# Kernel tuning notes

Measured on AMD Instinct MI355X. Metric: run time of the kernel, lower is better.

Reference implementation:

```python
import jax, jax.numpy as jnp
import numpy as np

N_NODES = 50000

def setup_inputs() -> dict:
    key = jax.random.key(0)
    k1, k2, k3, k4, k5 = jax.random.split(key, 5)
    feat = jax.random.normal(k1, (N_NODES, 192), dtype=jnp.float32)
    edge_feat = jax.random.normal(k2, (800000, 64), dtype=jnp.float32)
    src = jax.random.randint(k3, (800000,), 0, N_NODES, dtype=jnp.int32)
    dst = jax.random.randint(k4, (800000,), 0, N_NODES, dtype=jnp.int32)
    weight = jax.random.normal(k5, (256, 256), dtype=jnp.float32) * (1.0 / np.sqrt(256.0))
    bias = jnp.zeros((256,), dtype=jnp.float32)
    return {"feat": feat, "edge_feat": edge_feat, "src": src, "dst": dst,
            "weight": weight, "bias": bias}


def reference(feat, edge_feat, src, dst, weight, bias):
    N = feat.shape[0]
    ones_e = jnp.ones(src.shape[0], dtype=jnp.float32)
    # out-degree normalization of source features (pre-aggregation)
    out_deg = jnp.clip(jax.ops.segment_sum(ones_e, src, num_segments=N), 1.0, None)
    feat_n = feat * (out_deg ** -0.5)[:, None]            # [N, d_node]
    # message = concat(src_feat_norm, edge_feat); sum over dst.
    # segment_sum distributes over concat, so aggregate parts separately
    # (avoids materializing the [E, d_node+d_edge] message tensor).
    h_src = jax.ops.segment_sum(feat_n[src], dst, num_segments=N)   # [N, d_node]
    h_edge = jax.ops.segment_sum(edge_feat, dst, num_segments=N)    # [N, d_edge]
    h = jnp.concatenate([h_src, h_edge], axis=1)          # [N, in_feats]
    rst = h @ weight                                      # [N, out_feats]
    # in-degree normalization (post-aggregation)
    in_deg = jnp.clip(jax.ops.segment_sum(ones_e, dst, num_segments=N), 1.0, None)
    rst = rst * (in_deg ** -0.5)[:, None] + bias
    return rst
```

## Files before the change

### kernel.cpp

```cpp
#include <hip/hip_runtime.h>

#define NN 50000
#define NE 800000
#define DIN 256
#define DOUT 256

typedef __attribute__((ext_vector_type(8))) short bf16x8;
typedef __attribute__((ext_vector_type(8))) unsigned short u16x8;
typedef __attribute__((ext_vector_type(4))) float f32x4;

__device__ __forceinline__ unsigned short f2bf(float x) {
    unsigned int u = __builtin_bit_cast(unsigned int, x);
    u += 0x7fffu + ((u >> 16) & 1u);
    return (unsigned short)(u >> 16);
}
__device__ __forceinline__ float bf2f(unsigned short b) {
    return __builtin_bit_cast(float, ((unsigned int)b) << 16);
}


__global__ __launch_bounds__(256) void zero_meta(int* __restrict__ p, int n) {
    int i = blockIdx.x * 256 + threadIdx.x;
    if (i < n) p[i] = 0;
}

__global__ __launch_bounds__(256) void count_kernel(const int* __restrict__ src,
                                                    const int* __restrict__ dst,
                                                    int* __restrict__ in_cnt,
                                                    int* __restrict__ out_cnt) {
    int e = blockIdx.x * 256 + threadIdx.x;
    if (e < NE) {
        atomicAdd(in_cnt + dst[e], 1);
        atomicAdd(out_cnt + src[e], 1);
    }
}

__global__ __launch_bounds__(256) void scan1(const int* __restrict__ cnt,
                                             int* __restrict__ row_off,
                                             int* __restrict__ bsum) {
    __shared__ int tmp[256];
    int tid = threadIdx.x;
    int i = blockIdx.x * 256 + tid;
    int v = (i < NN) ? cnt[i] : 0;
    tmp[tid] = v;
    __syncthreads();
#pragma unroll
    for (int off = 1; off < 256; off <<= 1) {
        int t = (tid >= off) ? tmp[tid - off] : 0;
        __syncthreads();
        if (tid >= off) tmp[tid] += t;
        __syncthreads();
    }
    if (i < NN) row_off[i] = tmp[tid] - v;
    if (tid == 255) bsum[blockIdx.x] = tmp[255];
}

__global__ __launch_bounds__(256) void scan2(int* __restrict__ bsum, int nb) {
    __shared__ int tmp[256];
    int tid = threadIdx.x;
    int v = (tid < nb) ? bsum[tid] : 0;
    tmp[tid] = v;
    __syncthreads();
#pragma unroll
    for (int off = 1; off < 256; off <<= 1) {
        int t = (tid >= off) ? tmp[tid - off] : 0;
        __syncthreads();
        if (tid >= off) tmp[tid] += t;
        __syncthreads();
    }
    if (tid < nb) bsum[tid] = tmp[tid] - v;
}

__global__ __launch_bounds__(256) void scan3(int* __restrict__ row_off,
                                             int* __restrict__ cursor,
                                             float* __restrict__ odeg_inv,
                                             const int* __restrict__ out_cnt,
                                             const int* __restrict__ bsum) {
    int i = blockIdx.x * 256 + threadIdx.x;
    if (i < NN) {
        int v = row_off[i] + bsum[i >> 8];
        row_off[i] = v;
        cursor[i] = v;
        odeg_inv[i] = rsqrtf((float)max(out_cnt[i], 1));
    }
    if (i == NN) row_off[NN] = NE;
}

__global__ __launch_bounds__(256) void wconv(const float* __restrict__ W,
                                             unsigned short* __restrict__ wt) {
    int n = blockIdx.x, k = threadIdx.x;
    wt[n * 256 + k] = f2bf(W[k * 256 + n]);
}

__global__ __launch_bounds__(256) void featconv(const float* __restrict__ feat,
                                                const float* __restrict__ odeg_inv,
                                                unsigned short* __restrict__ featn) {
    int node = blockIdx.x * 4 + (threadIdx.x >> 6);
    int lane = threadIdx.x & 63;
    if (node >= NN || lane >= 48) return;
    float s = odeg_inv[node];
    float4 v = *(const float4*)(feat + (size_t)node * 192 + lane * 4);
    ushort4 o;
    o.x = f2bf(v.x * s); o.y = f2bf(v.y * s);
    o.z = f2bf(v.z * s); o.w = f2bf(v.w * s);
    *(ushort4*)(featn + (size_t)node * 192 + lane * 4) = o;
}

__global__ __launch_bounds__(256) void fill_kernel(const int* __restrict__ src,
                                                   const int* __restrict__ dst,
                                                   int* __restrict__ cursor,
                                                   int* __restrict__ perm,
                                                   unsigned short* __restrict__ eperm,
                                                   const float* __restrict__ edge_feat) {
    int tid = threadIdx.x;
    int e   = blockIdx.x * 16 + (tid >> 4);
    int sub = tid & 15;
    if (e >= NE) return;
    int pos = 0;
    if (sub == 0) {
        pos = atomicAdd(cursor + dst[e], 1);
        perm[pos] = src[e];
    }
    pos = __shfl(pos, 0, 16);
    float4 v = *(const float4*)(edge_feat + (size_t)e * 64 + sub * 4);
    ushort4 o;
    o.x = f2bf(v.x); o.y = f2bf(v.y); o.z = f2bf(v.z); o.w = f2bf(v.w);
    *(ushort4*)(eperm + (size_t)pos * 64 + sub * 4) = o;
}

__global__ __launch_bounds__(256) void aggregate_kernel(const unsigned short* __restrict__ featn,
                                                        const unsigned short* __restrict__ eperm,
                                                        const int* __restrict__ row_off,
                                                        const int* __restrict__ perm,
                                                        unsigned short* __restrict__ h_bf) {
    int node = blockIdx.x * 4 + (threadIdx.x >> 6);
    int lane = threadIdx.x & 63;
    if (node >= NN) return;
    int start = row_off[node];
    int end   = row_off[node + 1];

    int half = lane >> 5;
    int l    = lane & 31;
    bool isF = (l < 24);
    const unsigned short* fbase = featn + l * 8;
    const unsigned short* ebase = eperm + (l - 24) * 8;

    float acc[8];
#pragma unroll
    for (int k = 0; k < 8; ++k) acc[k] = 0.f;

    for (int i = start + half; i < end; i += 8) {
        int idx[4]; float w[4]; int s[4];
#pragma unroll
        for (int j = 0; j < 4; ++j) {
            int ii = i + 2 * j;
            idx[j] = min(ii, end - 1);
            w[j] = (ii < end) ? 1.f : 0.f;
        }
#pragma unroll
        for (int j = 0; j < 4; ++j) s[j] = perm[idx[j]];
        bf16x8 u[4];
#pragma unroll
        for (int j = 0; j < 4; ++j) {
            const unsigned short* p = isF ? (fbase + (size_t)s[j] * 192)
                                          : (ebase + (size_t)idx[j] * 64);
            u[j] = *(const bf16x8*)p;
        }
#pragma unroll
        for (int j = 0; j < 4; ++j) {
#pragma unroll
            for (int k = 0; k < 8; ++k)
                acc[k] = fmaf(bf2f((unsigned short)u[j][k]), w[j], acc[k]);
        }
    }

#pragma unroll
    for (int k = 0; k < 8; ++k) acc[k] += __shfl_xor(acc[k], 32);

    if (lane < 32) {
        u16x8 o;
#pragma unroll
        for (int k = 0; k < 8; ++k) o[k] = f2bf(acc[k]);
        *(u16x8*)(h_bf + (size_t)node * 256 + l * 8) = o;
    }
}

__global__ __launch_bounds__(256) void fill_fb(const int* __restrict__ src,
                                               const int* __restrict__ dst,
                                               int* __restrict__ cursor,
                                               int2* __restrict__ perm2) {
    int e = blockIdx.x * 256 + threadIdx.x;
    if (e < NE) {
        int d = dst[e];
        int pos = atomicAdd(cursor + d, 1);
        perm2[pos] = make_int2(e, src[e]);
    }
}

__global__ __launch_bounds__(256) void aggregate_fb(const unsigned short* __restrict__ featn,
                                                    const float* __restrict__ edge_feat,
                                                    const int* __restrict__ row_off,
                                                    const int2* __restrict__ perm2,
                                                    unsigned short* __restrict__ h_bf) {
    int node = blockIdx.x * 4 + (threadIdx.x >> 6);
    int lane = threadIdx.x & 63;
    if (node >= NN) return;
    int start = row_off[node];
    int end   = row_off[node + 1];

    float4 acc = make_float4(0.f, 0.f, 0.f, 0.f);

    if (lane < 48) {
        const unsigned short* fb = featn + lane * 4;
        for (int i = start; i < end; i += 8) {
            int2 p[8];
#pragma unroll
            for (int j = 0; j < 8; ++j) p[j] = perm2[min(i + j, end - 1)];
            ushort4 u[8];
#pragma unroll
            for (int j = 0; j < 8; ++j)
                u[j] = *(const ushort4*)(fb + (size_t)p[j].y * 192);
#pragma unroll
            for (int j = 0; j < 8; ++j) {
                float w = (i + j < end) ? 1.f : 0.f;
                acc.x = fmaf(bf2f(u[j].x), w, acc.x);
                acc.y = fmaf(bf2f(u[j].y), w, acc.y);
                acc.z = fmaf(bf2f(u[j].z), w, acc.z);
                acc.w = fmaf(bf2f(u[j].w), w, acc.w);
            }
        }
    } else {
        const float* eb = edge_feat + (lane - 48) * 4;
        for (int i = start; i < end; i += 8) {
            int2 p[8];
#pragma unroll
            for (int j = 0; j < 8; ++j) p[j] = perm2[min(i + j, end - 1)];
            float4 v[8];
#pragma unroll
            for (int j = 0; j < 8; ++j)
                v[j] = *(const float4*)(eb + (size_t)p[j].x * 64);
#pragma unroll
            for (int j = 0; j < 8; ++j) {
                float w = (i + j < end) ? 1.f : 0.f;
                acc.x = fmaf(v[j].x, w, acc.x);
                acc.y = fmaf(v[j].y, w, acc.y);
                acc.z = fmaf(v[j].z, w, acc.z);
                acc.w = fmaf(v[j].w, w, acc.w);
            }
        }
    }

    ushort4 o;
    o.x = f2bf(acc.x); o.y = f2bf(acc.y);
    o.z = f2bf(acc.z); o.w = f2bf(acc.w);
    *(ushort4*)(h_bf + (size_t)node * 256 + lane * 4) = o;
}

__global__ __launch_bounds__(256) void gemm_mfma(const unsigned short* __restrict__ h_bf,
                                                 const unsigned short* __restrict__ wt_bf,
                                                 const float* __restrict__ bias,
                                                 const int* __restrict__ row_off,
                                                 float* __restrict__ out) {
    int wave = threadIdx.x >> 6;
    int lane = threadIdx.x & 63;
    int m16  = lane & 15;
    int quad = lane >> 4;
    int rbase = blockIdx.x * 16;
    int cbase = wave * 64;

    const unsigned short* arow = h_bf + (size_t)(rbase + m16) * 256 + quad * 8;
    const unsigned short* b0p = wt_bf + (size_t)(cbase +  0 + m16) * 256 + quad * 8;
    const unsigned short* b1p = wt_bf + (size_t)(cbase + 16 + m16) * 256 + quad * 8;
    const unsigned short* b2p = wt_bf + (size_t)(cbase + 32 + m16) * 256 + quad * 8;
    const unsigned short* b3p = wt_bf + (size_t)(cbase + 48 + m16) * 256 + quad * 8;

    f32x4 acc0 = {0.f, 0.f, 0.f, 0.f};
    f32x4 acc1 = {0.f, 0.f, 0.f, 0.f};
    f32x4 acc2 = {0.f, 0.f, 0.f, 0.f};
    f32x4 acc3 = {0.f, 0.f, 0.f, 0.f};

#pragma unroll
    for (int k0 = 0; k0 < 256; k0 += 32) {
        bf16x8 a  = *(const bf16x8*)(arow + k0);
        bf16x8 b0 = *(const bf16x8*)(b0p + k0);
        bf16x8 b1 = *(const bf16x8*)(b1p + k0);
        bf16x8 b2 = *(const bf16x8*)(b2p + k0);
        bf16x8 b3 = *(const bf16x8*)(b3p + k0);
        acc0 = __builtin_amdgcn_mfma_f32_16x16x32_bf16(a, b0, acc0, 0, 0, 0);
        acc1 = __builtin_amdgcn_mfma_f32_16x16x32_bf16(a, b1, acc1, 0, 0, 0);
        acc2 = __builtin_amdgcn_mfma_f32_16x16x32_bf16(a, b2, acc2, 0, 0, 0);
        acc3 = __builtin_amdgcn_mfma_f32_16x16x32_bf16(a, b3, acc3, 0, 0, 0);
    }

    int grow0 = rbase + quad * 4;
    float s[4];
    int ro_prev = row_off[grow0];
#pragma unroll
    for (int r = 0; r < 4; ++r) {
        int nx = row_off[grow0 + r + 1];
        s[r] = rsqrtf((float)max(nx - ro_prev, 1));
        ro_prev = nx;
    }

    float bv0 = bias[cbase +  0 + m16];
    float bv1 = bias[cbase + 16 + m16];
    float bv2 = bias[cbase + 32 + m16];
    float bv3 = bias[cbase + 48 + m16];

#pragma unroll
    for (int r = 0; r < 4; ++r) {
        size_t rowoff = (size_t)(grow0 + r) * DOUT;
        out[rowoff + cbase +  0 + m16] = acc0[r] * s[r] + bv0;
        out[rowoff + cbase + 16 + m16] = acc1[r] * s[r] + bv1;
        out[rowoff + cbase + 32 + m16] = acc2[r] * s[r] + bv2;
        out[rowoff + cbase + 48 + m16] = acc3[r] * s[r] + bv3;
    }
}

extern "C" void kernel_launch(void* const* d_in, const int* in_sizes, int n_in,
                              void* d_out, int out_size, void* d_ws, size_t ws_size,
                              hipStream_t stream) {
    const float* feat      = (const float*)d_in[0];
    const float* edge_feat = (const float*)d_in[1];
    const int*   src       = (const int*)d_in[2];
    const int*   dst       = (const int*)d_in[3];
    const float* W         = (const float*)d_in[4];
    const float* bias      = (const float*)d_in[5];
    float* out = (float*)d_out;

    unsigned short* h_bf  = (unsigned short*)d_ws;
    unsigned short* wt_bf = h_bf + (size_t)NN * DIN;
    unsigned short* featn = wt_bf + 256 * 256;

    unsigned short* eperm = featn + (size_t)NN * 192;
    int*   perm_b     = (int*)(eperm + (size_t)NE * 64);
    int*   row_off_b  = perm_b + NE;
    float* odeg_inv_b = (float*)(row_off_b + NN + 2);
    int*   cursor_b   = (int*)(odeg_inv_b + NN);
    int*   bsum_b     = cursor_b + NN;
    size_t need = (size_t)((char*)(bsum_b + 256) - (char*)d_ws);

    int*   row_off_s  = (int*)(featn + (size_t)NN * 192);
    float* odeg_inv_s = (float*)(row_off_s + NN + 2);
    int*   cursor_s   = (int*)(odeg_inv_s + NN);
    int*   bsum_s     = cursor_s + NN;
    int2*  perm2      = (int2*)(bsum_s + 256);

    bool big_ws = (ws_size >= need);

    int*   row_off  = big_ws ? row_off_b  : row_off_s;
    float* odeg_inv = big_ws ? odeg_inv_b : odeg_inv_s;
    int*   cursor   = big_ws ? cursor_b   : cursor_s;
    int*   bsum     = big_ws ? bsum_b     : bsum_s;
    int*   in_cnt   = big_ws ? perm_b     : (int*)perm2;
    int*   out_cnt  = in_cnt + NN;

    const int SCAN_BLOCKS = (NN + 255) / 256;

    zero_meta<<<(2 * NN + 255) / 256, 256, 0, stream>>>(in_cnt, 2 * NN);
    count_kernel<<<(NE + 255) / 256, 256, 0, stream>>>(src, dst, in_cnt, out_cnt);
    scan1<<<SCAN_BLOCKS, 256, 0, stream>>>(in_cnt, row_off, bsum);
    scan2<<<1, 256, 0, stream>>>(bsum, SCAN_BLOCKS);
    scan3<<<(NN + 256) / 256, 256, 0, stream>>>(row_off, cursor, odeg_inv, out_cnt, bsum);
    wconv<<<256, 256, 0, stream>>>(W, wt_bf);
    if (big_ws) {
        fill_kernel<<<NE / 16, 256, 0, stream>>>(src, dst, cursor, perm_b,
                                                 eperm, edge_feat);
        featconv<<<(NN + 3) / 4, 256, 0, stream>>>(feat, odeg_inv, featn);
        aggregate_kernel<<<(NN + 3) / 4, 256, 0, stream>>>(featn, eperm, row_off,
                                                           perm_b, h_bf);
    } else {
        featconv<<<(NN + 3) / 4, 256, 0, stream>>>(feat, odeg_inv, featn);
        fill_fb<<<(NE + 255) / 256, 256, 0, stream>>>(src, dst, cursor, perm2);
        aggregate_fb<<<(NN + 3) / 4, 256, 0, stream>>>(featn, edge_feat, row_off,
                                                       perm2, h_bf);
    }
    gemm_mfma<<<NN / 16, 256, 0, stream>>>(h_bf, wt_bf, bias, row_off, out);
}
```

Measured before the change: 546.8 us.

## Fuse aggregation with MFMA GEMM via LDS tile of aggregated rows

```diff
diff --git a/kernel.cpp b/kernel.cpp
--- a/kernel.cpp
+++ b/kernel.cpp
@@ -4,6 +4,8 @@
 #define NE 800000
 #define DIN 256
 #define DOUT 256
+
+#define LDS_STRIDE 264
 
 typedef __attribute__((ext_vector_type(8))) short bf16x8;
 typedef __attribute__((ext_vector_type(8))) unsigned short u16x8;
@@ -128,16 +130,18 @@
     *(ushort4*)(eperm + (size_t)pos * 64 + sub * 4) = o;
 }
 
-__global__ __launch_bounds__(256) void aggregate_kernel(const unsigned short* __restrict__ featn,
-                                                        const unsigned short* __restrict__ eperm,
-                                                        const int* __restrict__ row_off,
-                                                        const int* __restrict__ perm,
-                                                        unsigned short* __restrict__ h_bf) {
-    int node = blockIdx.x * 4 + (threadIdx.x >> 6);
+__global__ __launch_bounds__(256) void agg_gemm(const unsigned short* __restrict__ featn,
+                                                const unsigned short* __restrict__ eperm,
+                                                const int* __restrict__ row_off,
+                                                const int* __restrict__ perm,
+                                                const unsigned short* __restrict__ wt_bf,
+                                                const float* __restrict__ bias,
+                                                float* __restrict__ out) {
+    __shared__ unsigned short hlds[16 * LDS_STRIDE];
+
+    int wave = threadIdx.x >> 6;
     int lane = threadIdx.x & 63;
-    if (node >= NN) return;
-    int start = row_off[node];
-    int end   = row_off[node + 1];
+    int rbase = blockIdx.x * 16;
 
     int half = lane >> 5;
     int l    = lane & 31;
@@ -145,43 +149,103 @@
     const unsigned short* fbase = featn + l * 8;
     const unsigned short* ebase = eperm + (l - 24) * 8;
 
-    float acc[8];
-#pragma unroll
-    for (int k = 0; k < 8; ++k) acc[k] = 0.f;
-
-    for (int i = start + half; i < end; i += 8) {
-        int idx[4]; float w[4]; int s[4];
-#pragma unroll
-        for (int j = 0; j < 4; ++j) {
-            int ii = i + 2 * j;
-            idx[j] = min(ii, end - 1);
-            w[j] = (ii < end) ? 1.f : 0.f;
+    for (int c = 0; c < 4; ++c) {
+        int node = rbase + wave * 4 + c;
+        int start = row_off[node];
+        int end   = row_off[node + 1];
+
+        float acc[8];
+#pragma unroll
+        for (int k = 0; k < 8; ++k) acc[k] = 0.f;
+
+        for (int i = start + half; i < end; i += 8) {
+            int idx[4]; float w[4]; int s[4];
+#pragma unroll
+            for (int j = 0; j < 4; ++j) {
+                int ii = i + 2 * j;
+                idx[j] = min(ii, end - 1);
+                w[j] = (ii < end) ? 1.f : 0.f;
+            }
+#pragma unroll
+            for (int j = 0; j < 4; ++j) s[j] = perm[idx[j]];
+            bf16x8 u[4];
+#pragma unroll
+            for (int j = 0; j < 4; ++j) {
+                const unsigned short* p = isF ? (fbase + (size_t)s[j] * 192)
+                                              : (ebase + (size_t)idx[j] * 64);
+                u[j] = *(const bf16x8*)p;
+            }
+#pragma unroll
+            for (int j = 0; j < 4; ++j) {
+#pragma unroll
+                for (int k = 0; k < 8; ++k)
+                    acc[k] = fmaf(bf2f((unsigned short)u[j][k]), w[j], acc[k]);
+            }
         }
-#pragma unroll
-        for (int j = 0; j < 4; ++j) s[j] = perm[idx[j]];
-        bf16x8 u[4];
-#pragma unroll
-        for (int j = 0; j < 4; ++j) {
-            const unsigned short* p = isF ? (fbase + (size_t)s[j] * 192)
-                                          : (ebase + (size_t)idx[j] * 64);
-            u[j] = *(const bf16x8*)p;
+
+#pragma unroll
+        for (int k = 0; k < 8; ++k) acc[k] += __shfl_xor(acc[k], 32);
+
+        if (lane < 32) {
+            u16x8 o;
+#pragma unroll
+            for (int k = 0; k < 8; ++k) o[k] = f2bf(acc[k]);
+            *(u16x8*)(hlds + (wave * 4 + c) * LDS_STRIDE + l * 8) = o;
         }
-#pragma unroll
-        for (int j = 0; j < 4; ++j) {
-#pragma unroll
-            for (int k = 0; k < 8; ++k)
-                acc[k] = fmaf(bf2f((unsigned short)u[j][k]), w[j], acc[k]);
-        }
-    }
-
-#pragma unroll
-    for (int k = 0; k < 8; ++k) acc[k] += __shfl_xor(acc[k], 32);
-
-    if (lane < 32) {
-        u16x8 o;
-#pragma unroll
-        for (int k = 0; k < 8; ++k) o[k] = f2bf(acc[k]);
-        *(u16x8*)(h_bf + (size_t)node * 256 + l * 8) = o;
+    }
+
+    __syncthreads();
+
+    int m16  = lane & 15;
+    int quad = lane >> 4;
+    int cbase = wave * 64;
+
+    const unsigned short* arow = hlds + m16 * LDS_STRIDE + quad * 8;
+    const unsigned short* b0p = wt_bf + (size_t)(cbase +  0 + m16) * 256 + quad * 8;
+    const unsigned short* b1p = wt_bf + (size_t)(cbase + 16 + m16) * 256 + quad * 8;
+    const unsigned short* b2p = wt_bf + (size_t)(cbase + 32 + m16) * 256 + quad * 8;
+    const unsigned short* b3p = wt_bf + (size_t)(cbase + 48 + m16) * 256 + quad * 8;
+
+    f32x4 acc0 = {0.f, 0.f, 0.f, 0.f};
+    f32x4 acc1 = {0.f, 0.f, 0.f, 0.f};
+    f32x4 acc2 = {0.f, 0.f, 0.f, 0.f};
+    f32x4 acc3 = {0.f, 0.f, 0.f, 0.f};
+
+#pragma unroll
+    for (int k0 = 0; k0 < 256; k0 += 32) {
+        bf16x8 a  = *(const bf16x8*)(arow + k0);
+        bf16x8 b0 = *(const bf16x8*)(b0p + k0);
+        bf16x8 b1 = *(const bf16x8*)(b1p + k0);
+        bf16x8 b2 = *(const bf16x8*)(b2p + k0);
+        bf16x8 b3 = *(const bf16x8*)(b3p + k0);
+        acc0 = __builtin_amdgcn_mfma_f32_16x16x32_bf16(a, b0, acc0, 0, 0, 0);
+        acc1 = __builtin_amdgcn_mfma_f32_16x16x32_bf16(a, b1, acc1, 0, 0, 0);
+        acc2 = __builtin_amdgcn_mfma_f32_16x16x32_bf16(a, b2, acc2, 0, 0, 0);
+        acc3 = __builtin_amdgcn_mfma_f32_16x16x32_bf16(a, b3, acc3, 0, 0, 0);
+    }
+
+    int grow0 = rbase + quad * 4;
+    float s[4];
+    int ro_prev = row_off[grow0];
+#pragma unroll
+    for (int r = 0; r < 4; ++r) {
+        int nx = row_off[grow0 + r + 1];
+        s[r] = rsqrtf((float)max(nx - ro_prev, 1));
+        ro_prev = nx;
+    }
+
+    float bv0 = bias[cbase +  0 + m16];
+    float bv1 = bias[cbase + 16 + m16];
+    float bv2 = bias[cbase + 32 + m16];
+    float bv3 = bias[cbase + 48 + m16];
+
+#pragma unroll
+    for (int r = 0; r < 4; ++r) {
+        size_t rowoff = (size_t)(grow0 + r) * DOUT;
+        out[rowoff + cbase +  0 + m16] = acc0[r] * s[r] + bv0;
+        out[rowoff + cbase + 16 + m16] = acc1[r] * s[r] + bv1;
+        out[rowoff + cbase + 32 + m16] = acc2[r] * s[r] + bv2;
+        out[rowoff + cbase + 48 + m16] = acc3[r] * s[r] + bv3;
     }
 }
 
@@ -367,13 +431,13 @@
         fill_kernel<<<NE / 16, 256, 0, stream>>>(src, dst, cursor, perm_b,
                                                  eperm, edge_feat);
         featconv<<<(NN + 3) / 4, 256, 0, stream>>>(feat, odeg_inv, featn);
-        aggregate_kernel<<<(NN + 3) / 4, 256, 0, stream>>>(featn, eperm, row_off,
-                                                           perm_b, h_bf);
+        agg_gemm<<<NN / 16, 256, 0, stream>>>(featn, eperm, row_off, perm_b,
+                                              wt_bf, bias, out);
     } else {
         featconv<<<(NN + 3) / 4, 256, 0, stream>>>(feat, odeg_inv, featn);
         fill_fb<<<(NE + 255) / 256, 256, 0, stream>>>(src, dst, cursor, perm2);
         aggregate_fb<<<(NN + 3) / 4, 256, 0, stream>>>(featn, edge_feat, row_off,
                                                        perm2, h_bf);
-    }
-    gemm_mfma<<<NN / 16, 256, 0, stream>>>(h_bf, wt_bf, bias, row_off, out);
-}
+        gemm_mfma<<<NN / 16, 256, 0, stream>>>(h_bf, wt_bf, bias, row_off, out);
+    }
+}
```

After: 536.9 us. Within noise of the previous version (-1.8%).
